# Kernel optimization log

Measured on AMD Instinct MI355X. Metric: run time of the kernel, lower is better.

## Reference

```python
import jax, jax.numpy as jnp
import numpy as np

N_NODES = 100000


def sage_conv(x, src, dst, counts, Wl, bl, Wr):
    # mean-aggregate source features into destination nodes
    msg_sum = jax.ops.segment_sum(x[src], dst, num_segments=N_NODES)  # [N, d]
    aggr = msg_sum / counts  # zero-degree nodes stay 0 (counts clamped to 1)
    return aggr @ Wl + bl + x @ Wr


def setup_inputs() -> dict:
    key = jax.random.key(0)
    ks = jax.random.split(key, 16)
    N, E, IN, H, OUT = N_NODES, 640000, 128, 128, 40
    x = jax.random.normal(ks[0], (N, IN), dtype=jnp.float32)
    edge_index = jax.random.randint(ks[1], (2, E), 0, N, dtype=jnp.int64)

    def lin(k, fan_in, fan_out):
        s = 1.0 / np.sqrt(fan_in)
        return jax.random.uniform(k, (fan_in, fan_out), jnp.float32, -s, s)

    return {
        "x": x,
        "edge_index": edge_index,
        "W1l": lin(ks[2], IN, H), "b1": jnp.zeros((H,), jnp.float32), "W1r": lin(ks[3], IN, H),
        "W2l": lin(ks[4], H, H), "b2": jnp.zeros((H,), jnp.float32), "W2r": lin(ks[5], H, H),
        "W3l": lin(ks[6], H, H), "b3": jnp.zeros((H,), jnp.float32), "W3r": lin(ks[7], H, H),
        "Wf1": lin(ks[8], H, H), "bf1": jnp.zeros((H,), jnp.float32),
        "Wf2": lin(ks[9], H, OUT), "bf2": jnp.zeros((OUT,), jnp.float32),
    }


def reference(x, edge_index, W1l, b1, W1r, W2l, b2, W2r, W3l, b3, W3r, Wf1, bf1, Wf2, bf2):
    src, dst = edge_index[0], edge_index[1]
    counts = jax.ops.segment_sum(jnp.ones_like(dst, dtype=x.dtype), dst,
                                 num_segments=N_NODES)
    counts = jnp.maximum(counts, 1.0)[:, None]  # [N, 1]

    h = jax.nn.relu(sage_conv(x, src, dst, counts, W1l, b1, W1r))
    h = jax.nn.relu(sage_conv(h, src, dst, counts, W2l, b2, W2r))
    h = sage_conv(h, src, dst, counts, W3l, b3, W3r)

    z = jax.nn.relu(h @ Wf1 + bf1) @ Wf2 + bf2  # [N, out]
    return jax.nn.log_softmax(z, axis=1), h
```

## Files before the change

### kernel.cpp

```cpp
#include <hip/hip_runtime.h>
#include <math.h>

#define N_NODES 100000
#define HDIM    128
#define ODIM    40
#define NBLK    ((N_NODES + 255) / 256)

typedef unsigned short u16;
typedef unsigned int   u32;
typedef short bf16x8 __attribute__((ext_vector_type(8)));
typedef float f32x4  __attribute__((ext_vector_type(4)));

__device__ inline float bf16lo_to_f(u32 v) {
    u32 u = v << 16; float f; __builtin_memcpy(&f, &u, 4); return f;
}
__device__ inline float bf16hi_to_f(u32 v) {
    u32 u = v & 0xffff0000u; float f; __builtin_memcpy(&f, &u, 4); return f;
}
__device__ inline u16 f_to_bf16(float f) {
    u32 u; __builtin_memcpy(&u, &f, 4);
    u32 r = (u + 0x7fffu + ((u >> 16) & 1u)) >> 16;
    return (u16)r;
}
__device__ inline u32 pack_bf16x2(float a, float b) {
    return (u32)f_to_bf16(a) | ((u32)f_to_bf16(b) << 16);
}

__global__ __launch_bounds__(256) void count_deg_kernel(
    const int* __restrict__ dst, int* __restrict__ ic, int E)
{
    int e = blockIdx.x * 256 + threadIdx.x;
    if (e < E) atomicAdd(ic + dst[e], 1);
}

__global__ __launch_bounds__(256) void block_sum_kernel(
    const int* __restrict__ ic, int* __restrict__ bs, int n)
{
    __shared__ int sm[256];
    int t = threadIdx.x;
    int i = blockIdx.x * 256 + t;
    sm[t] = (i < n) ? ic[i] : 0;
    __syncthreads();
    for (int s = 128; s > 0; s >>= 1) {
        if (t < s) sm[t] += sm[t + s];
        __syncthreads();
    }
    if (t == 0) bs[blockIdx.x] = sm[0];
}

__global__ __launch_bounds__(512) void scan_bs_kernel(int* __restrict__ bs, int nb)
{
    __shared__ int sm[512];
    int t = threadIdx.x;
    sm[t] = (t < nb) ? bs[t] : 0;
    __syncthreads();
    for (int off = 1; off < 512; off <<= 1) {
        int v = (t >= off) ? sm[t - off] : 0;
        __syncthreads();
        sm[t] += v;
        __syncthreads();
    }
    if (t < nb) bs[t] = (t == 0) ? 0 : sm[t - 1];
}

__global__ __launch_bounds__(256) void scan_block_kernel(
    const int* __restrict__ ic, const int* __restrict__ bs,
    int* __restrict__ pc, int n)
{
    __shared__ int sm[256];
    int t = threadIdx.x;
    int i = blockIdx.x * 256 + t;
    int v = (i < n) ? ic[i] : 0;
    sm[t] = v;
    __syncthreads();
    for (int off = 1; off < 256; off <<= 1) {
        int u = (t >= off) ? sm[t - off] : 0;
        __syncthreads();
        sm[t] += u;
        __syncthreads();
    }
    if (i < n) pc[i] = bs[blockIdx.x] + sm[t] - v;
}

__global__ __launch_bounds__(256) void fill_kernel(
    const int* __restrict__ src, const int* __restrict__ dst,
    int* __restrict__ pc, int* __restrict__ cs, int E)
{
    int e = blockIdx.x * 256 + threadIdx.x;
    if (e < E) {
        int p = atomicAdd(pc + dst[e], 1);
        cs[p] = src[e];
    }
}

struct WPtrs { const float* w[7]; };

#define PREP_F2BF  25000
#define PREP_PACKW (PREP_F2BF + 448)
#define PREP_WF2   (PREP_PACKW + 24)
#define PREP_ZERO  (PREP_WF2 + 392)

__global__ __launch_bounds__(256) void prep_kernel(
    const float2* __restrict__ x2, u32* __restrict__ X32,
    WPtrs p, u16* __restrict__ Wpk,
    const float* __restrict__ Wf2, u16* __restrict__ Wf2p,
    int* __restrict__ ic)
{
    const int b = blockIdx.x;
    const int tid = threadIdx.x;
    if (b < PREP_F2BF) {
        int i = b * 256 + tid;
        float2 v = x2[i];
        X32[i] = pack_bf16x2(v.x, v.y);
    } else if (b < PREP_PACKW) {
        int bb = b - PREP_F2BF;
        int mat = bb >> 6;
        int e = (bb & 63) * 256 + tid;
        int k = e >> 7, n = e & 127;
        float v = p.w[mat][e];
        int nt = n >> 4, ks = k >> 5, q = (k >> 3) & 3, j = k & 7;
        Wpk[mat * 16384 + (((nt * 4 + ks) * 64 + q * 16 + (n & 15)) << 3) + j] = f_to_bf16(v);
    } else if (b < PREP_WF2) {
        int e = (b - PREP_PACKW) * 256 + tid;
        if (e < 128 * 48) {
            int k = e / 48, n = e - k * 48;
            float v = (n < ODIM) ? Wf2[k * ODIM + n] : 0.f;
            int nt = n >> 4, ks = k >> 5, q = (k >> 3) & 3, j = k & 7;
            Wf2p[(((nt * 4 + ks) * 64 + q * 16 + (n & 15)) << 3) + j] = f_to_bf16(v);
        }
    } else {
        int i = (b - PREP_WF2) * 256 + tid;
        if (i < 100352) ic[i] = 0;
    }
}

__global__ __launch_bounds__(256) void gather_mean_grp_kernel(
    const u32* __restrict__ feat,
    const int* __restrict__ cs, const int* __restrict__ pc, const int* __restrict__ ic,
    u32* __restrict__ A)
{
    const int grp  = threadIdx.x >> 4;
    const int ch   = threadIdx.x & 15;
    const int node = blockIdx.x * 16 + grp;
    const int end  = pc[node];
    const int deg  = ic[node];
    const int start = end - deg;

    const u32* fb = feat + (ch << 2);

    float acc[8] = {0.f,0.f,0.f,0.f,0.f,0.f,0.f,0.f};
    const uint4 Z = {0u, 0u, 0u, 0u};

    if (deg > 0) {
        uint4 c0 = *reinterpret_cast<const uint4*>(fb + ((size_t)cs[start] << 6));
        uint4 c1 = (deg > 1)
            ? *reinterpret_cast<const uint4*>(fb + ((size_t)cs[start + 1] << 6)) : Z;
        for (int j = 0; j < deg; ++j) {
            uint4 n = (j + 2 < deg)
                ? *reinterpret_cast<const uint4*>(fb + ((size_t)cs[start + j + 2] << 6)) : Z;
            acc[0] += bf16lo_to_f(c0.x); acc[1] += bf16hi_to_f(c0.x);
            acc[2] += bf16lo_to_f(c0.y); acc[3] += bf16hi_to_f(c0.y);
            acc[4] += bf16lo_to_f(c0.z); acc[5] += bf16hi_to_f(c0.z);
            acc[6] += bf16lo_to_f(c0.w); acc[7] += bf16hi_to_f(c0.w);
            c0 = c1; c1 = n;
        }
    }

    float inv = 1.0f / (float)(deg > 0 ? deg : 1);
    uint4 o;
    o.x = pack_bf16x2(acc[0] * inv, acc[1] * inv);
    o.y = pack_bf16x2(acc[2] * inv, acc[3] * inv);
    o.z = pack_bf16x2(acc[4] * inv, acc[5] * inv);
    o.w = pack_bf16x2(acc[6] * inv, acc[7] * inv);
    *reinterpret_cast<uint4*>(A + ((size_t)node << 6) + (ch << 2)) = o;
}

__device__ inline void stage_w(const u16* __restrict__ Wp, u16* __restrict__ sDst,
                               int wave, int lane, int nchunk4)
{
    for (int it = 0; it < nchunk4; ++it) {
        int off = (it * 4 + wave) << 9;
        __builtin_amdgcn_global_load_lds(
            (const __attribute__((address_space(1))) void*)(Wp + off + (lane << 3)),
            (__attribute__((address_space(3))) void*)(sDst + off), 16, 0, 0);
    }
}

__device__ inline void stage_w8(const u16* __restrict__ Wp, u16* __restrict__ sDst,
                                int wave, int lane)
{
    #pragma unroll
    for (int it = 0; it < 4; ++it) {
        int off = (it * 8 + wave) << 9;
        __builtin_amdgcn_global_load_lds(
            (const __attribute__((address_space(1))) void*)(Wp + off + (lane << 3)),
            (__attribute__((address_space(3))) void*)(sDst + off), 16, 0, 0);
    }
}

__global__ __launch_bounds__(512) void mfma_gemm_kernel(
    const u16* __restrict__ A1, const u16* __restrict__ A2,
    const u16* __restrict__ W1p, const u16* __restrict__ W2p,
    const float* __restrict__ bias,
    u16* __restrict__ out16, float* __restrict__ out32, int do_relu)
{
    __shared__ __align__(16) u16 sW[32768];
    const int tid  = threadIdx.x;
    const int wave = tid >> 6;
    const int lane = tid & 63;
    const int m = lane & 15;
    const int q = lane >> 4;
    const int base = blockIdx.x * 128;

    int row = base + wave * 16 + m; if (row > N_NODES - 1) row = N_NODES - 1;

    bf16x8 a[4], c[4];
    #pragma unroll
    for (int ks = 0; ks < 4; ++ks) {
        a[ks] = *reinterpret_cast<const bf16x8*>(A1 + ((size_t)row << 7) + ((ks * 4 + q) << 3));
        c[ks] = *reinterpret_cast<const bf16x8*>(A2 + ((size_t)row << 7) + ((ks * 4 + q) << 3));
    }
    stage_w8(W1p, sW, wave, lane);
    stage_w8(W2p, sW + 16384, wave, lane);
    __syncthreads();

    f32x4 acc[8];
    #pragma unroll
    for (int nt = 0; nt < 8; ++nt) acc[nt] = (f32x4){0.f, 0.f, 0.f, 0.f};

    #pragma unroll
    for (int ks = 0; ks < 4; ++ks) {
        #pragma unroll
        for (int nt = 0; nt < 8; ++nt) {
            bf16x8 b = *reinterpret_cast<const bf16x8*>(sW + (((nt * 4 + ks) * 64 + lane) << 3));
            acc[nt] = __builtin_amdgcn_mfma_f32_16x16x32_bf16(a[ks], b, acc[nt], 0, 0, 0);
        }
    }
    #pragma unroll
    for (int ks = 0; ks < 4; ++ks) {
        #pragma unroll
        for (int nt = 0; nt < 8; ++nt) {
            bf16x8 b = *reinterpret_cast<const bf16x8*>(sW + 16384 + (((nt * 4 + ks) * 64 + lane) << 3));
            acc[nt] = __builtin_amdgcn_mfma_f32_16x16x32_bf16(c[ks], b, acc[nt], 0, 0, 0);
        }
    }
    __syncthreads();

    if (out32) {
        #pragma unroll
        for (int nt = 0; nt < 8; ++nt) {
            int col = nt * 16 + m;
            float bv = bias[col];
            #pragma unroll
            for (int r = 0; r < 4; ++r) {
                int rg = base + wave * 16 + q * 4 + r;
                if (rg < N_NODES) out32[((size_t)rg << 7) + col] = acc[nt][r] + bv;
            }
        }
    }

    if (out16) {
        #pragma unroll
        for (int nt = 0; nt < 8; ++nt) {
            int col = nt * 16 + m;
            float bv = bias[col];
            #pragma unroll
            for (int r = 0; r < 4; ++r) {
                float v = acc[nt][r] + bv;
                if (do_relu) v = fmaxf(v, 0.f);
                int rl = wave * 16 + q * 4 + r;
                sW[rl * 136 + col] = f_to_bf16(v);
            }
        }
        __syncthreads();
        #pragma unroll
        for (int it = 0; it < 4; ++it) {
            int cc = it * 512 + tid;
            int rowl = cc >> 4, ch = cc & 15;
            int rowg = base + rowl;
            if (rowg < N_NODES)
                *reinterpret_cast<uint4*>(out16 + ((size_t)rowg << 7) + (ch << 3)) =
                    *reinterpret_cast<const uint4*>(sW + rowl * 136 + (ch << 3));
        }
    }
}

__global__ __launch_bounds__(256) void mfma_head_kernel(
    const u16* __restrict__ h3,
    const u16* __restrict__ Wf1p, const float* __restrict__ bf1,
    const u16* __restrict__ Wf2p, const float* __restrict__ bf2,
    float* __restrict__ out)
{
    __shared__ __align__(16) u16 sW1[16384];
    __shared__ __align__(16) u16 sW2[6144];
    const int tid  = threadIdx.x;
    const int wave = tid >> 6;
    const int lane = tid & 63;
    const int m = lane & 15;
    const int q = lane >> 4;
    const int base = blockIdx.x * 128;

    int row0 = base + wave * 16 + m;       if (row0 > N_NODES - 1) row0 = N_NODES - 1;
    int row1 = base + 64 + wave * 16 + m;  if (row1 > N_NODES - 1) row1 = N_NODES - 1;

    bf16x8 a0[4], a1[4];
    #pragma unroll
    for (int ks = 0; ks < 4; ++ks) {
        a0[ks] = *reinterpret_cast<const bf16x8*>(h3 + ((size_t)row0 << 7) + ((ks * 4 + q) << 3));
        a1[ks] = *reinterpret_cast<const bf16x8*>(h3 + ((size_t)row1 << 7) + ((ks * 4 + q) << 3));
    }
    stage_w(Wf1p, sW1, wave, lane, 8);
    stage_w(Wf2p, sW2, wave, lane, 3);
    __syncthreads();

    f32x4 acc0[8], acc1[8];
    #pragma unroll
    for (int nt = 0; nt < 8; ++nt) {
        acc0[nt] = (f32x4){0.f, 0.f, 0.f, 0.f};
        acc1[nt] = (f32x4){0.f, 0.f, 0.f, 0.f};
    }
    #pragma unroll
    for (int ks = 0; ks < 4; ++ks) {
        #pragma unroll
        for (int nt = 0; nt < 8; ++nt) {
            bf16x8 b = *reinterpret_cast<const bf16x8*>(sW1 + (((nt * 4 + ks) * 64 + lane) << 3));
            acc0[nt] = __builtin_amdgcn_mfma_f32_16x16x32_bf16(a0[ks], b, acc0[nt], 0, 0, 0);
            acc1[nt] = __builtin_amdgcn_mfma_f32_16x16x32_bf16(a1[ks], b, acc1[nt], 0, 0, 0);
        }
    }
    __syncthreads();

    #pragma unroll
    for (int nt = 0; nt < 8; ++nt) {
        int col = nt * 16 + m;
        float bv = bf1[col];
        #pragma unroll
        for (int r = 0; r < 4; ++r) {
            int dc = (wave * 4 + (nt >> 1)) * 64 + ((nt & 1) * 2 + (m >> 3)) * 16 + (q * 4 + r);
            sW1[(dc << 3) | (m & 7)]          = f_to_bf16(fmaxf(acc0[nt][r] + bv, 0.f));
            sW1[8192 + ((dc << 3) | (m & 7))] = f_to_bf16(fmaxf(acc1[nt][r] + bv, 0.f));
        }
    }
    __syncthreads();

    f32x4 ca[3], cb[3];
    #pragma unroll
    for (int nt = 0; nt < 3; ++nt) {
        ca[nt] = (f32x4){0.f, 0.f, 0.f, 0.f};
        cb[nt] = (f32x4){0.f, 0.f, 0.f, 0.f};
    }
    #pragma unroll
    for (int ks = 0; ks < 4; ++ks) {
        bf16x8 t0 = *reinterpret_cast<const bf16x8*>(sW1 + (((wave * 4 + ks) * 64 + lane) << 3));
        bf16x8 t1 = *reinterpret_cast<const bf16x8*>(sW1 + 8192 + (((wave * 4 + ks) * 64 + lane) << 3));
        #pragma unroll
        for (int nt = 0; nt < 3; ++nt) {
            bf16x8 b = *reinterpret_cast<const bf16x8*>(sW2 + (((nt * 4 + ks) * 64 + lane) << 3));
            ca[nt] = __builtin_amdgcn_mfma_f32_16x16x32_bf16(t0, b, ca[nt], 0, 0, 0);
            cb[nt] = __builtin_amdgcn_mfma_f32_16x16x32_bf16(t1, b, cb[nt], 0, 0, 0);
        }
    }

    #pragma unroll
    for (int tile = 0; tile < 2; ++tile) {
        const f32x4* acc2 = tile ? cb : ca;
        float z[3][4];
        float mx[4] = {-INFINITY, -INFINITY, -INFINITY, -INFINITY};
        #pragma unroll
        for (int nt = 0; nt < 3; ++nt) {
            int col = nt * 16 + m;
            bool valid = (col < ODIM);
            float bv = valid ? bf2[col] : 0.f;
            #pragma unroll
            for (int r = 0; r < 4; ++r) {
                z[nt][r] = acc2[nt][r] + bv;
                if (valid) mx[r] = fmaxf(mx[r], z[nt][r]);
            }
        }
        #pragma unroll
        for (int off = 1; off < 16; off <<= 1) {
            #pragma unroll
            for (int r = 0; r < 4; ++r) mx[r] = fmaxf(mx[r], __shfl_xor(mx[r], off, 16));
        }
        float sum[4] = {0.f, 0.f, 0.f, 0.f};
        #pragma unroll
        for (int nt = 0; nt < 3; ++nt) {
            int col = nt * 16 + m;
            if (col < ODIM) {
                #pragma unroll
                for (int r = 0; r < 4; ++r) sum[r] += expf(z[nt][r] - mx[r]);
            }
        }
        #pragma unroll
        for (int off = 1; off < 16; off <<= 1) {
            #pragma unroll
            for (int r = 0; r < 4; ++r) sum[r] += __shfl_xor(sum[r], off, 16);
        }
        float lse[4];
        #pragma unroll
        for (int r = 0; r < 4; ++r) lse[r] = logf(sum[r]) + mx[r];

        int rowbase = base + tile * 64 + wave * 16;
        #pragma unroll
        for (int nt = 0; nt < 3; ++nt) {
            int col = nt * 16 + m;
            if (col >= ODIM) continue;
            #pragma unroll
            for (int r = 0; r < 4; ++r) {
                int rowg = rowbase + q * 4 + r;
                if (rowg < N_NODES) out[(size_t)rowg * ODIM + col] = z[nt][r] - lse[r];
            }
        }
    }
}

extern "C" void kernel_launch(void* const* d_in, const int* in_sizes, int n_in,
                              void* d_out, int out_size, void* d_ws, size_t ws_size,
                              hipStream_t stream) {
    const float* x   = (const float*)d_in[0];
    const int*   ei  = (const int*)d_in[1];
    const int E = in_sizes[1] / 2;
    const int* src = ei;
    const int* dst = ei + E;

    const float* W1l = (const float*)d_in[2];
    const float* b1  = (const float*)d_in[3];
    const float* W1r = (const float*)d_in[4];
    const float* W2l = (const float*)d_in[5];
    const float* b2  = (const float*)d_in[6];
    const float* W2r = (const float*)d_in[7];
    const float* W3l = (const float*)d_in[8];
    const float* b3  = (const float*)d_in[9];
    const float* W3r = (const float*)d_in[10];
    const float* Wf1 = (const float*)d_in[11];
    const float* bf1 = (const float*)d_in[12];
    const float* Wf2 = (const float*)d_in[13];
    const float* bf2 = (const float*)d_in[14];

    float* out     = (float*)d_out;
    float* outTail = out + (size_t)N_NODES * ODIM;

    int* ic = (int*)out;
    int* pc = ic + 100352;
    int* bs = pc + 100352;
    int* cs = bs + 1024;

    const size_t FEAT16 = (size_t)N_NODES * HDIM;
    u16* X16  = (u16*)d_ws;
    u16* F16a = X16  + FEAT16;
    u16* F16b = F16a + FEAT16;
    u16* A16  = F16b + FEAT16;
    u16* Wpk  = A16  + FEAT16;
    u16* Wp_1l = Wpk + 0 * 16384;
    u16* Wp_1r = Wpk + 1 * 16384;
    u16* Wp_2l = Wpk + 2 * 16384;
    u16* Wp_2r = Wpk + 3 * 16384;
    u16* Wp_3l = Wpk + 4 * 16384;
    u16* Wp_3r = Wpk + 5 * 16384;
    u16* Wp_f1 = Wpk + 6 * 16384;
    u16* Wf2p  = Wpk + 7 * 16384;

    const int gemmGrid   = (N_NODES + 127) / 128;
    const int gatherGrid = N_NODES / 16;
    const int edgeGrid   = (E + 255) / 256;

    WPtrs wp; wp.w[0] = W1l; wp.w[1] = W1r; wp.w[2] = W2l; wp.w[3] = W2r;
    wp.w[4] = W3l; wp.w[5] = W3r; wp.w[6] = Wf1;
    prep_kernel<<<PREP_ZERO, 256, 0, stream>>>(
        (const float2*)x, (u32*)X16, wp, Wpk, Wf2, Wf2p, ic);

    count_deg_kernel<<<edgeGrid, 256, 0, stream>>>(dst, ic, E);
    block_sum_kernel<<<NBLK, 256, 0, stream>>>(ic, bs, N_NODES);
    scan_bs_kernel<<<1, 512, 0, stream>>>(bs, NBLK);
    scan_block_kernel<<<NBLK, 256, 0, stream>>>(ic, bs, pc, N_NODES);
    fill_kernel<<<edgeGrid, 256, 0, stream>>>(src, dst, pc, cs, E);

    gather_mean_grp_kernel<<<gatherGrid, 256, 0, stream>>>((const u32*)X16, cs, pc, ic, (u32*)A16);
    mfma_gemm_kernel<<<gemmGrid, 512, 0, stream>>>(A16, X16, Wp_1l, Wp_1r, b1, F16a, nullptr, 1);

    gather_mean_grp_kernel<<<gatherGrid, 256, 0, stream>>>((const u32*)F16a, cs, pc, ic, (u32*)A16);
    mfma_gemm_kernel<<<gemmGrid, 512, 0, stream>>>(A16, F16a, Wp_2l, Wp_2r, b2, F16b, nullptr, 1);

    gather_mean_grp_kernel<<<gatherGrid, 256, 0, stream>>>((const u32*)F16b, cs, pc, ic, (u32*)A16);
    mfma_gemm_kernel<<<gemmGrid, 512, 0, stream>>>(A16, F16b, Wp_3l, Wp_3r, b3, F16a, outTail, 0);

    mfma_head_kernel<<<gemmGrid, 256, 0, stream>>>(F16a, Wp_f1, bf1, Wf2p, bf2, out);
}
```

Baseline: 389.8 us.

## Process two 128-row tiles per GEMM block to amortize weight staging

Each GEMM block now covers 256 rows instead of 128. It loads A rows for both tiles up front and reuses the LDS-staged weights for both, which halves the number of weight loads into LDS across the grid. The bf16 output goes through a separate small LDS buffer in four 32-row chunks, each with a pair of barriers, instead of reusing the weight buffer. In exchange it uses more registers, adds launch_bounds occupancy hints and more syncs, and launches half as many blocks (391), which is close to the CU count.

```diff
diff --git a/kernel.cpp b/kernel.cpp
--- a/kernel.cpp
+++ b/kernel.cpp
@@ -198,89 +198,103 @@
     }
 }
 
-__global__ __launch_bounds__(512) void mfma_gemm_kernel(
+__global__ __launch_bounds__(512, 4) void mfma_gemm_kernel(
     const u16* __restrict__ A1, const u16* __restrict__ A2,
     const u16* __restrict__ W1p, const u16* __restrict__ W2p,
     const float* __restrict__ bias,
     u16* __restrict__ out16, float* __restrict__ out32, int do_relu)
 {
     __shared__ __align__(16) u16 sW[32768];
+    __shared__ __align__(16) u16 sOut[32 * 136];
     const int tid  = threadIdx.x;
     const int wave = tid >> 6;
     const int lane = tid & 63;
     const int m = lane & 15;
     const int q = lane >> 4;
-    const int base = blockIdx.x * 128;
-
-    int row = base + wave * 16 + m; if (row > N_NODES - 1) row = N_NODES - 1;
-
-    bf16x8 a[4], c[4];
+    const int base = blockIdx.x * 256;
+
+    int r0 = base + wave * 16 + m;        if (r0 > N_NODES - 1) r0 = N_NODES - 1;
+    int r1 = base + 128 + wave * 16 + m;  if (r1 > N_NODES - 1) r1 = N_NODES - 1;
+
+    bf16x8 a0[4], c0[4], a1[4], c1[4];
     #pragma unroll
     for (int ks = 0; ks < 4; ++ks) {
-        a[ks] = *reinterpret_cast<const bf16x8*>(A1 + ((size_t)row << 7) + ((ks * 4 + q) << 3));
-        c[ks] = *reinterpret_cast<const bf16x8*>(A2 + ((size_t)row << 7) + ((ks * 4 + q) << 3));
+        a0[ks] = *reinterpret_cast<const bf16x8*>(A1 + ((size_t)r0 << 7) + ((ks * 4 + q) << 3));
+        c0[ks] = *reinterpret_cast<const bf16x8*>(A2 + ((size_t)r0 << 7) + ((ks * 4 + q) << 3));
+        a1[ks] = *reinterpret_cast<const bf16x8*>(A1 + ((size_t)r1 << 7) + ((ks * 4 + q) << 3));
+        c1[ks] = *reinterpret_cast<const bf16x8*>(A2 + ((size_t)r1 << 7) + ((ks * 4 + q) << 3));
     }
     stage_w8(W1p, sW, wave, lane);
     stage_w8(W2p, sW + 16384, wave, lane);
     __syncthreads();
 
-    f32x4 acc[8];
-    #pragma unroll
-    for (int nt = 0; nt < 8; ++nt) acc[nt] = (f32x4){0.f, 0.f, 0.f, 0.f};
-
-    #pragma unroll
-    for (int ks = 0; ks < 4; ++ks) {
-        #pragma unroll
-        for (int nt = 0; nt < 8; ++nt) {
-            bf16x8 b = *reinterpret_cast<const bf16x8*>(sW + (((nt * 4 + ks) * 64 + lane) << 3));
-            acc[nt] = __builtin_amdgcn_mfma_f32_16x16x32_bf16(a[ks], b, acc[nt], 0, 0, 0);
-        }
-    }
-    #pragma unroll
-    for (int ks = 0; ks < 4; ++ks) {
-        #pragma unroll
-        for (int nt = 0; nt < 8; ++nt) {
-            bf16x8 b = *reinterpret_cast<const bf16x8*>(sW + 16384 + (((nt * 4 + ks) * 64 + lane) << 3));
-            acc[nt] = __builtin_amdgcn_mfma_f32_16x16x32_bf16(c[ks], b, acc[nt], 0, 0, 0);
-        }
-    }
-    __syncthreads();
-
-    if (out32) {
-        #pragma unroll
-        for (int nt = 0; nt < 8; ++nt) {
-            int col = nt * 16 + m;
-            float bv = bias[col];
-            #pragma unroll
-            for (int r = 0; r < 4; ++r) {
-                int rg = base + wave * 16 + q * 4 + r;
-                if (rg < N_NODES) out32[((size_t)rg << 7) + col] = acc[nt][r] + bv;
-            }
-        }
-    }
-
-    if (out16) {
-        #pragma unroll
-        for (int nt = 0; nt < 8; ++nt) {
-            int col = nt * 16 + m;
-            float bv = bias[col];
-            #pragma unroll
-            for (int r = 0; r < 4; ++r) {
-                float v = acc[nt][r] + bv;
-                if (do_relu) v = fmaxf(v, 0.f);
-                int rl = wave * 16 + q * 4 + r;
-                sW[rl * 136 + col] = f_to_bf16(v);
-            }
-        }
-        __syncthreads();
-        #pragma unroll
-        for (int it = 0; it < 4; ++it) {
-            int cc = it * 512 + tid;
-            int rowl = cc >> 4, ch = cc & 15;
-            int rowg = base + rowl;
-            if (rowg < N_NODES)
-                *reinterpret_cast<uint4*>(out16 + ((size_t)rowg << 7) + (ch << 3)) =
-                    *reinterpret_cast<const uint4*>(sW + rowl * 136 + (ch << 3));
+    #pragma unroll
+    for (int tile = 0; tile < 2; ++tile) {
+        f32x4 acc[8];
+        #pragma unroll
+        for (int nt = 0; nt < 8; ++nt) acc[nt] = (f32x4){0.f, 0.f, 0.f, 0.f};
+
+        #pragma unroll
+        for (int ks = 0; ks < 4; ++ks) {
+            bf16x8 a = tile ? a1[ks] : a0[ks];
+            #pragma unroll
+            for (int nt = 0; nt < 8; ++nt) {
+                bf16x8 b = *reinterpret_cast<const bf16x8*>(sW + (((nt * 4 + ks) * 64 + lane) << 3));
+                acc[nt] = __builtin_amdgcn_mfma_f32_16x16x32_bf16(a, b, acc[nt], 0, 0, 0);
+            }
+        }
+        #pragma unroll
+        for (int ks = 0; ks < 4; ++ks) {
+            bf16x8 c = tile ? c1[ks] : c0[ks];
+            #pragma unroll
+            for (int nt = 0; nt < 8; ++nt) {
+                bf16x8 b = *reinterpret_cast<const bf16x8*>(sW + 16384 + (((nt * 4 + ks) * 64 + lane) << 3));
+                acc[nt] = __builtin_amdgcn_mfma_f32_16x16x32_bf16(c, b, acc[nt], 0, 0, 0);
+            }
+        }
+
+        const int tbase = base + tile * 128;
+
+        if (out32) {
+            #pragma unroll
+            for (int nt = 0; nt < 8; ++nt) {
+                int col = nt * 16 + m;
+                float bv = bias[col];
+                #pragma unroll
+                for (int r = 0; r < 4; ++r) {
+                    int rg = tbase + wave * 16 + q * 4 + r;
+                    if (rg < N_NODES) out32[((size_t)rg << 7) + col] = acc[nt][r] + bv;
+                }
+            }
+        }
+
+        if (out16) {
+            #pragma unroll
+            for (int h = 0; h < 4; ++h) {
+                if ((wave >> 1) == h) {
+                    #pragma unroll
+                    for (int nt = 0; nt < 8; ++nt) {
+                        int col = nt * 16 + m;
+                        float bv = bias[col];
+                        #pragma unroll
+                        for (int r = 0; r < 4; ++r) {
+                            float v = acc[nt][r] + bv;
+                            if (do_relu) v = fmaxf(v, 0.f);
+                            int rl = (wave & 1) * 16 + q * 4 + r;
+                            sOut[rl * 136 + col] = f_to_bf16(v);
+                        }
+                    }
+                }
+                __syncthreads();
+                {
+                    int row = tid >> 4, ch = tid & 15;
+                    int rowg = tbase + h * 32 + row;
+                    if (rowg < N_NODES)
+                        *reinterpret_cast<uint4*>(out16 + ((size_t)rowg << 7) + (ch << 3)) =
+                            *reinterpret_cast<const uint4*>(sOut + row * 136 + (ch << 3));
+                }
+                __syncthreads();
+            }
         }
     }
 }
@@ -460,7 +474,8 @@
     u16* Wp_f1 = Wpk + 6 * 16384;
     u16* Wf2p  = Wpk + 7 * 16384;
 
-    const int gemmGrid   = (N_NODES + 127) / 128;
+    const int gemmGrid   = (N_NODES + 255) / 256;
+    const int headGrid   = (N_NODES + 127) / 128;
     const int gatherGrid = N_NODES / 16;
     const int edgeGrid   = (E + 255) / 256;
 
@@ -484,5 +499,5 @@
     gather_mean_grp_kernel<<<gatherGrid, 256, 0, stream>>>((const u32*)F16b, cs, pc, ic, (u32*)A16);
     mfma_gemm_kernel<<<gemmGrid, 512, 0, stream>>>(A16, F16b, Wp_3l, Wp_3r, b3, F16a, outTail, 0);
 
-    mfma_head_kernel<<<gemmGrid, 256, 0, stream>>>(F16a, Wp_f1, bf1, Wf2p, bf2, out);
-}
+    mfma_head_kernel<<<headGrid, 256, 0, stream>>>(F16a, Wp_f1, bf1, Wf2p, bf2, out);
+}
```

Result: slower. 400.8 us (+2.8%).
